# Kernel optimization log

Hardware: AMD Instinct MI355X
Metric: run time of the kernel (lower is better)

## Reference

```python
import jax, jax.numpy as jnp
import numpy as np

B, C, H = 16, 256, 32          # batch, in_channels(=out_channels), image_size
HEADS, HS = 8, 32              # heads = out_channels // head_size
D = HEADS * HS                 # head_dim = 256
N = H * H                      # tokens = 1024
EPS = 1e-5


def _rel_indices(h, w):
    # Faithful port of RelativeAttention2d.get_indices
    y = np.arange(h)
    x = np.arange(w)
    y1, x1, y2, x2 = np.meshgrid(y, x, y, x, indexing='ij')
    idx = (y1 - y2 + h - 1) * (2 * w - 1) + (x1 - x2 + w - 1)
    return jnp.asarray(idx.reshape(-1), dtype=jnp.int32)  # [N*N]


def setup_inputs() -> dict:
    key = jax.random.key(0)
    ks = jax.random.split(key, 10)
    s = 0.02
    return {
        'x': jax.random.normal(ks[0], (B, C, H, H), jnp.float32),
        'ln_g': jnp.ones((C,), jnp.float32),
        'ln_b': jnp.zeros((C,), jnp.float32),
        'wq': jax.random.normal(ks[1], (D, C), jnp.float32) * s,
        'bq': jnp.zeros((D,), jnp.float32),
        'wk': jax.random.normal(ks[2], (D, C), jnp.float32) * s,
        'bk': jnp.zeros((D,), jnp.float32),
        'wv': jax.random.normal(ks[3], (D, C), jnp.float32) * s,
        'bv': jnp.zeros((D,), jnp.float32),
        'wo': jax.random.normal(ks[4], (C, D), jnp.float32) * s,
        'bo': jnp.zeros((C,), jnp.float32),
        'rel_bias': jax.random.normal(ks[5], (HEADS, (2 * H - 1) * (2 * H - 1)), jnp.float32),
        'rel_idx': _rel_indices(H, H),
    }


def reference(x, ln_g, ln_b, wq, bq, wk, bk, wv, bv, wo, bo, rel_bias, rel_idx):
    b = x.shape[0]
    # norm(): LayerNorm over channel axis (dim 1 after the double transpose)
    mu = jnp.mean(x, axis=1, keepdims=True)
    var = jnp.mean((x - mu) ** 2, axis=1, keepdims=True)
    xn = (x - mu) / jnp.sqrt(var + EPS)
    xn = xn * ln_g[None, :, None, None] + ln_b[None, :, None, None]
    # reshape_for_linear: raw reshape [b, C, H, W] -> [b, N, C] (as in torch)
    xr = xn.reshape(b, N, C)
    # projections, then raw view(b, heads, head_size, -1) as in torch
    q = (xr @ wq.T + bq).reshape(b, HEADS, HS, N)
    k = (xr @ wk.T + bk).reshape(b, HEADS, HS, N)
    v = (xr @ wv.T + bv).reshape(b, HEADS, HS, N)
    # dots = k^T q / sqrt(head_dim)   [b, heads, N, N]
    dots = jnp.einsum('bhdn,bhdm->bhnm', k, q) / np.float32(np.sqrt(D))
    # gathered relative position bias  [heads, N, N]
    bias = rel_bias[:, rel_idx].reshape(HEADS, N, N)
    attn = jax.nn.softmax(dots + bias[None], axis=-2)  # non-standard softmax dim
    # out = v @ attn  [b, heads, head_size, N]
    out = jnp.einsum('bhdn,bhnm->bhdm', v, attn)
    out = out.reshape(b, H, H, D)  # raw view as in torch
    out = out @ wo.T + bo          # to_output linear (dropout is identity in eval)
    out = out.reshape(b, C, H, H)  # raw view back to [b, out_channels, H, W]
    return x + out
```

## Files before the change

### kernel.cpp

```cpp
#include <hip/hip_runtime.h>
#include <cstdint>

#define PERB 262144

typedef __attribute__((ext_vector_type(8))) short bf16x8;
typedef __attribute__((ext_vector_type(4))) float f32x4;
typedef unsigned short ushort_t;

__device__ __forceinline__ uint16_t f2bf(float f) {
    uint32_t u = __float_as_uint(f);
    u += 0x7fff + ((u >> 16) & 1);
    return (uint16_t)(u >> 16);
}

__global__ __launch_bounds__(256) void wcvt_kernel(
    const float* __restrict__ wq, const float* __restrict__ wk,
    const float* __restrict__ wv, const float* __restrict__ wo,
    ushort_t* __restrict__ oq, ushort_t* __restrict__ ok,
    ushort_t* __restrict__ ov, ushort_t* __restrict__ oo)
{
    const int which = blockIdx.x >> 6;
    const int idx = ((blockIdx.x & 63) * 256 + threadIdx.x) * 4;
    const float* src = which == 0 ? wq : which == 1 ? wk : which == 2 ? wv : wo;
    ushort_t* dst    = which == 0 ? oq : which == 1 ? ok : which == 2 ? ov : oo;
    const float4 v = *(const float4*)&src[idx];
    uint2 p;
    p.x = (uint32_t)f2bf(v.x) | ((uint32_t)f2bf(v.y) << 16);
    p.y = (uint32_t)f2bf(v.z) | ((uint32_t)f2bf(v.w) << 16);
    *(uint2*)&dst[idx] = p;
}

__global__ __launch_bounds__(256) void ln_kernel(
    const float* __restrict__ x, const float* __restrict__ gam,
    const float* __restrict__ bet, ushort_t* __restrict__ X)
{
    const int blk = blockIdx.x;
    const int b   = blk >> 4;
    const int sp0 = (blk & 15) << 6;
    const int tid = threadIdx.x;
    const int spl = tid & 63;
    const int cg  = tid >> 6;
    const int c0  = cg << 6;
    const int sp  = sp0 + spl;
    const float* xb = x + (size_t)b * PERB + sp;

    float vals[64];
    float s = 0.f, sq = 0.f;
#pragma unroll
    for (int i = 0; i < 64; ++i) {
        float v = xb[(size_t)(c0 + i) * 1024];
        vals[i] = v; s += v; sq += v * v;
    }
    __shared__ float rs[4][64];
    __shared__ float rq[4][64];
    rs[cg][spl] = s; rq[cg][spl] = sq;
    __syncthreads();
    const float ts = rs[0][spl] + rs[1][spl] + rs[2][spl] + rs[3][spl];
    const float tq = rq[0][spl] + rq[1][spl] + rq[2][spl] + rq[3][spl];
    const float mean = ts * (1.f / 256.f);
    const float var  = tq * (1.f / 256.f) - mean * mean;
    const float rstd = rsqrtf(var + 1e-5f);

    ushort_t* Xb = X + (size_t)b * PERB + sp;
#pragma unroll
    for (int i = 0; i < 64; ++i) {
        const int c = c0 + i;
        Xb[(size_t)c * 1024] = f2bf((vals[i] - mean) * rstd * gam[c] + bet[c]);
    }
}

__global__ __launch_bounds__(256, 3) void qkv_kernel(
    const ushort_t* __restrict__ X,
    const ushort_t* __restrict__ wq, const float* __restrict__ bq,
    const ushort_t* __restrict__ wk, const float* __restrict__ bk,
    const ushort_t* __restrict__ wv, const float* __restrict__ bv,
    ushort_t* __restrict__ Q, ushort_t* __restrict__ K, ushort_t* __restrict__ V)
{
    __shared__ __align__(16) ushort_t Xl[512 * 8];
    __shared__ __align__(16) ushort_t Wl[3][512 * 8];

    const int blk = blockIdx.x;
    const int m0  = (blk >> 2) << 6;
    const int n0  = (blk & 3) << 6;
    const int tid = threadIdx.x;
    const int w    = tid >> 6;
    const int lane = tid & 63;
    const int quad = lane >> 4;
    const int c    = lane & 15;

    f32x4 acc[3][4];
#pragma unroll
    for (int o3 = 0; o3 < 3; ++o3)
#pragma unroll
        for (int i = 0; i < 4; ++i) acc[o3][i] = (f32x4){0.f, 0.f, 0.f, 0.f};

    for (int kc = 0; kc < 4; ++kc) {
        const int k0 = kc << 6;
        __syncthreads();
#pragma unroll
        for (int i = 0; i < 2; ++i) {
            const int id = tid + i * 256;
            const int kq = id >> 6, m = id & 63;
            *(bf16x8*)&Xl[id * 8] = *(const bf16x8*)&X[(size_t)(m0 + m) * 256 + k0 + kq * 8];
        }
#pragma unroll
        for (int i = 0; i < 2; ++i) {
            const int id = tid + i * 256;
            const int kq = id >> 6, n = id & 63;
            const size_t g = (size_t)(n0 + n) * 256 + k0 + kq * 8;
            *(bf16x8*)&Wl[0][id * 8] = *(const bf16x8*)&wq[g];
            *(bf16x8*)&Wl[1][id * 8] = *(const bf16x8*)&wk[g];
            *(bf16x8*)&Wl[2][id * 8] = *(const bf16x8*)&wv[g];
        }
        __syncthreads();
#pragma unroll
        for (int ks = 0; ks < 2; ++ks) {
            const int kq = ks * 4 + quad;
            bf16x8 af[4];
#pragma unroll
            for (int msub = 0; msub < 4; ++msub)
                af[msub] = *(const bf16x8*)&Xl[(kq * 64 + msub * 16 + c) * 8];
            bf16x8 bw[3];
#pragma unroll
            for (int o3 = 0; o3 < 3; ++o3)
                bw[o3] = *(const bf16x8*)&Wl[o3][(kq * 64 + w * 16 + c) * 8];
#pragma unroll
            for (int o3 = 0; o3 < 3; ++o3)
#pragma unroll
                for (int msub = 0; msub < 4; ++msub)
                    acc[o3][msub] = __builtin_amdgcn_mfma_f32_16x16x32_bf16(
                        bw[o3], af[msub], acc[o3][msub], 0, 0, 0);
        }
    }

    const int n = n0 + w * 16 + quad * 4;
    const float4 bq4 = *(const float4*)&bq[n];
    const float4 bk4 = *(const float4*)&bk[n];
    const float4 bv4 = *(const float4*)&bv[n];
    ushort_t* outs[3] = {Q, K, V};
    const float4 bias[3] = {bq4, bk4, bv4};
#pragma unroll
    for (int msub = 0; msub < 4; ++msub) {
        const size_t m = (size_t)(m0 + msub * 16 + c);
#pragma unroll
        for (int o3 = 0; o3 < 3; ++o3) {
            const f32x4 a = acc[o3][msub];
            uint2 p;
            p.x = (uint32_t)f2bf(a[0] + bias[o3].x) | ((uint32_t)f2bf(a[1] + bias[o3].y) << 16);
            p.y = (uint32_t)f2bf(a[2] + bias[o3].z) | ((uint32_t)f2bf(a[3] + bias[o3].w) << 16);
            *(uint2*)&outs[o3][m * 256 + n] = p;
        }
    }
}

__global__ __launch_bounds__(256, 3) void attn_kernel(
    const ushort_t* __restrict__ Q, const ushort_t* __restrict__ K,
    const ushort_t* __restrict__ V, const float* __restrict__ relb,
    ushort_t* __restrict__ O)
{
    __shared__ __align__(16) unsigned char smem[29184];
    char* Pbase = (char*)smem;
    char* Kbase = (char*)smem + 18432;
    char* Vbase = (char*)smem + 22528;
    float* red  = (float*)(smem + 27136);

    const int blk = blockIdx.x;
    const int bh  = blk & 127;
    const int mt  = blk >> 7;
    const int b   = bh >> 3;
    const int h   = bh & 7;
    const int m0  = mt << 7;
    const int tid = threadIdx.x;
    const int w    = tid >> 6;
    const int lane = tid & 63;
    const int quad = lane >> 4;
    const int c    = lane & 15;

    const size_t base = (size_t)b * PERB + (size_t)h * 32768;
    const ushort_t* Qb = Q + base;
    const ushort_t* Kb = K + base;
    const ushort_t* Vb = V + base;
    const float* rbh = relb + h * 3969;

    {
        const int mm = tid & 127;
        const int sg = tid >> 7;
        union { bf16x8 v; uint16_t u[8]; } g0, g1;
#pragma unroll
        for (int j = 0; j < 8; ++j)
            g0.u[j] = Qb[(size_t)(sg * 16 + j) * 1024 + m0 + mm];
#pragma unroll
        for (int j = 0; j < 8; ++j)
            g1.u[j] = Qb[(size_t)(sg * 16 + 8 + j) * 1024 + m0 + mm];
        *(bf16x8*)(Pbase + (sg * 2 + 0) * 2048 + mm * 16) = g0.v;
        *(bf16x8*)(Pbase + (sg * 2 + 1) * 2048 + mm * 16) = g1.v;
    }
    __syncthreads();
    bf16x8 qfrag[8];
#pragma unroll
    for (int msub = 0; msub < 8; ++msub)
        qfrag[msub] = *(const bf16x8*)(Pbase + quad * 2048 + (msub * 16 + c) * 16);

    int my[8], mx[8];
#pragma unroll
    for (int msub = 0; msub < 8; ++msub) {
        const int m = m0 + msub * 16 + c;
        my[msub] = m >> 5; mx[msub] = m & 31;
    }

    f32x4 oacc[2][2];
#pragma unroll
    for (int i = 0; i < 2; ++i)
#pragma unroll
        for (int j = 0; j < 2; ++j)
            oacc[i][j] = (f32x4){0.f, 0.f, 0.f, 0.f};
    float dsum[8];
#pragma unroll
    for (int i = 0; i < 8; ++i) dsum[i] = 0.f;

    const int knn = tid & 63, ksg = (tid >> 6) & 3;
    const int vs = tid >> 3, vng = tid & 7;

    for (int ch = 0; ch < 16; ++ch) {
        const int n0c = ch << 6;
        __syncthreads();

        {
            union { bf16x8 v; uint16_t u[8]; } g;
#pragma unroll
            for (int j = 0; j < 8; ++j)
                g.u[j] = Kb[(size_t)(ksg * 8 + j) * 1024 + n0c + knn];
            *(bf16x8*)(Kbase + ksg * 1024 + knn * 16) = g.v;
        }
        *(bf16x8*)(Vbase + vs * 144 + vng * 16) =
            *(const bf16x8*)&Vb[(size_t)vs * 1024 + n0c + vng * 8];
        __syncthreads();

        const bf16x8 kf = *(const bf16x8*)(Kbase + quad * 1024 + (w * 16 + c) * 16);
        f32x4 sacc[8];
#pragma unroll
        for (int msub = 0; msub < 8; ++msub) {
            const f32x4 z = {0.f, 0.f, 0.f, 0.f};
            sacc[msub] = __builtin_amdgcn_mfma_f32_16x16x32_bf16(kf, qfrag[msub], z, 0, 0, 0);
        }
        const int nb = n0c + w * 16 + quad * 4;
#pragma unroll
        for (int msub = 0; msub < 8; ++msub) {
            uint32_t pk[2];
            float ps[4];
#pragma unroll
            for (int r = 0; r < 4; ++r) {
                const int n  = nb + r;
                const int dy = (n >> 5) - my[msub] + 31;
                const int dx = (n & 31) - mx[msub] + 31;
                const float sc = sacc[msub][r] * 0.0625f + rbh[dy * 63 + dx];
                const float p  = __expf(sc);
                ps[r] = p;
                dsum[msub] += p;
            }
            pk[0] = (uint32_t)f2bf(ps[0]) | ((uint32_t)f2bf(ps[1]) << 16);
            pk[1] = (uint32_t)f2bf(ps[2]) | ((uint32_t)f2bf(ps[3]) << 16);
            *(uint32_t*)(Pbase + (msub * 16 + c) * 144 + (w * 16 + quad * 4) * 2 + 0) = pk[0];
            *(uint32_t*)(Pbase + (msub * 16 + c) * 144 + (w * 16 + quad * 4) * 2 + 4) = pk[1];
        }
        __syncthreads();

#pragma unroll
        for (int kstep = 0; kstep < 2; ++kstep) {
            const bf16x8 vf0 = *(const bf16x8*)(Vbase + (0 * 16 + c) * 144 + kstep * 64 + quad * 16);
            const bf16x8 vf1 = *(const bf16x8*)(Vbase + (1 * 16 + c) * 144 + kstep * 64 + quad * 16);
#pragma unroll
            for (int mi = 0; mi < 2; ++mi) {
                const int msub = w * 2 + mi;
                const bf16x8 pf = *(const bf16x8*)(Pbase + (msub * 16 + c) * 144 + kstep * 64 + quad * 16);
                oacc[0][mi] = __builtin_amdgcn_mfma_f32_16x16x32_bf16(vf0, pf, oacc[0][mi], 0, 0, 0);
                oacc[1][mi] = __builtin_amdgcn_mfma_f32_16x16x32_bf16(vf1, pf, oacc[1][mi], 0, 0, 0);
            }
        }
    }

    __syncthreads();
#pragma unroll
    for (int msub = 0; msub < 8; ++msub) {
        float v = dsum[msub];
        v += __shfl_xor(v, 16, 64);
        v += __shfl_xor(v, 32, 64);
        if (quad == 0) red[w * 128 + msub * 16 + c] = v;
    }
    __syncthreads();

    ushort_t* Ob = O + base;
#pragma unroll
    for (int mi = 0; mi < 2; ++mi) {
        const int msub = w * 2 + mi;
        const float dtot = red[0 * 128 + msub * 16 + c] + red[1 * 128 + msub * 16 + c]
                         + red[2 * 128 + msub * 16 + c] + red[3 * 128 + msub * 16 + c];
        const float inv = 1.0f / dtot;
        const int m = m0 + msub * 16 + c;
#pragma unroll
        for (int ssub = 0; ssub < 2; ++ssub) {
#pragma unroll
            for (int r = 0; r < 4; ++r) {
                const int s = ssub * 16 + quad * 4 + r;
                Ob[(size_t)s * 1024 + m] = f2bf(oacc[ssub][mi][r] * inv);
            }
        }
    }
}

__global__ __launch_bounds__(256, 4) void oproj_kernel(
    const ushort_t* __restrict__ A, const ushort_t* __restrict__ wo,
    const float* __restrict__ bo, const float* __restrict__ x,
    float* __restrict__ out)
{
    __shared__ __align__(16) ushort_t Al[512 * 8];
    __shared__ __align__(16) ushort_t Wl[512 * 8];

    const int blk = blockIdx.x;
    const int m0  = (blk >> 2) << 6;
    const int n0  = (blk & 3) << 6;
    const int tid = threadIdx.x;
    const int w    = tid >> 6;
    const int lane = tid & 63;
    const int quad = lane >> 4;
    const int c    = lane & 15;

    f32x4 acc[4];
#pragma unroll
    for (int i = 0; i < 4; ++i) acc[i] = (f32x4){0.f, 0.f, 0.f, 0.f};

    for (int kc = 0; kc < 4; ++kc) {
        const int k0 = kc << 6;
        __syncthreads();
#pragma unroll
        for (int i = 0; i < 2; ++i) {
            const int id = tid + i * 256;
            const int kq = id >> 6, mn = id & 63;
            *(bf16x8*)&Al[id * 8] = *(const bf16x8*)&A [(size_t)(m0 + mn) * 256 + k0 + kq * 8];
            *(bf16x8*)&Wl[id * 8] = *(const bf16x8*)&wo[(size_t)(n0 + mn) * 256 + k0 + kq * 8];
        }
        __syncthreads();
#pragma unroll
        for (int ks = 0; ks < 2; ++ks) {
            const int kq = ks * 4 + quad;
            const bf16x8 bw = *(const bf16x8*)&Wl[(kq * 64 + w * 16 + c) * 8];
#pragma unroll
            for (int msub = 0; msub < 4; ++msub) {
                const bf16x8 af = *(const bf16x8*)&Al[(kq * 64 + msub * 16 + c) * 8];
                acc[msub] = __builtin_amdgcn_mfma_f32_16x16x32_bf16(bw, af, acc[msub], 0, 0, 0);
            }
        }
    }

    const int n = n0 + w * 16 + quad * 4;
    const float4 bo4 = *(const float4*)&bo[n];
#pragma unroll
    for (int msub = 0; msub < 4; ++msub) {
        const size_t g = (size_t)(m0 + msub * 16 + c) * 256 + n;
        const float4 r = *(const float4*)&x[g];
        float4 t;
        t.x = acc[msub][0] + bo4.x + r.x;
        t.y = acc[msub][1] + bo4.y + r.y;
        t.z = acc[msub][2] + bo4.z + r.z;
        t.w = acc[msub][3] + bo4.w + r.w;
        *(float4*)&out[g] = t;
    }
}

extern "C" void kernel_launch(void* const* d_in, const int* in_sizes, int n_in,
                              void* d_out, int out_size, void* d_ws, size_t ws_size,
                              hipStream_t stream)
{
    (void)in_sizes; (void)n_in; (void)out_size; (void)ws_size;
    const float* x   = (const float*)d_in[0];
    const float* lng = (const float*)d_in[1];
    const float* lnb = (const float*)d_in[2];
    const float* wq  = (const float*)d_in[3];
    const float* bq  = (const float*)d_in[4];
    const float* wk  = (const float*)d_in[5];
    const float* bk  = (const float*)d_in[6];
    const float* wv  = (const float*)d_in[7];
    const float* bv  = (const float*)d_in[8];
    const float* wo  = (const float*)d_in[9];
    const float* bo  = (const float*)d_in[10];
    const float* rb  = (const float*)d_in[11];

    ushort_t* ws = (ushort_t*)d_ws;
    ushort_t* Xbf = ws;
    ushort_t* Qbf = ws + 1 * 4194304;
    ushort_t* Kbf = ws + 2 * 4194304;
    ushort_t* Vbf = ws + 3 * 4194304;
    ushort_t* Obf = ws + 4 * 4194304;
    ushort_t* Wqb = ws + 5 * 4194304;
    ushort_t* Wkb = Wqb + 65536;
    ushort_t* Wvb = Wkb + 65536;
    ushort_t* Wob = Wvb + 65536;
    float* out = (float*)d_out;

    hipLaunchKernelGGL(wcvt_kernel,  dim3(256),  dim3(256), 0, stream,
                       wq, wk, wv, wo, Wqb, Wkb, Wvb, Wob);
    hipLaunchKernelGGL(ln_kernel,    dim3(256),  dim3(256), 0, stream, x, lng, lnb, Xbf);
    hipLaunchKernelGGL(qkv_kernel,   dim3(1024), dim3(256), 0, stream,
                       Xbf, Wqb, bq, Wkb, bk, Wvb, bv, Qbf, Kbf, Vbf);
    hipLaunchKernelGGL(attn_kernel,  dim3(1024), dim3(256), 0, stream, Qbf, Kbf, Vbf, rb, Obf);
    hipLaunchKernelGGL(oproj_kernel, dim3(1024), dim3(256), 0, stream, Obf, Wob, bo, x, out);
}
```

Measured before the change: 188.2 us.

## Restructure attention loop: register prefetch, LDS bias table, exp2, MFMA row sums

The attention kernel now stages the per-head relative bias table into LDS, pre-scaled by log2(e), and replaces expf with exp2 of an fma. K and V tiles for the next chunk are prefetched into registers while the current chunk computes, and V is double-buffered so one barrier per chunk is dropped. P and V use XOR-swizzled LDS layouts instead of padded rows. The softmax denominator now comes from an extra MFMA against a ones vector instead of per-thread sums with shuffle and LDS reduction. P is rounded to bf16 by truncation instead of round-to-nearest, which costs a little accuracy. LDS use grows to about 44.5 KB per block, which may limit how many blocks fit per CU.

```diff
diff --git a/kernel.cpp b/kernel.cpp
--- a/kernel.cpp
+++ b/kernel.cpp
@@ -153,16 +153,19 @@
     }
 }
 
+#define C1F 0.09016844005556022f
+#define LOG2EF 1.4426950408889634f
+
 __global__ __launch_bounds__(256, 3) void attn_kernel(
     const ushort_t* __restrict__ Q, const ushort_t* __restrict__ K,
     const ushort_t* __restrict__ V, const float* __restrict__ relb,
     ushort_t* __restrict__ O)
 {
-    __shared__ __align__(16) unsigned char smem[29184];
-    char* Pbase = (char*)smem;
-    char* Kbase = (char*)smem + 18432;
-    char* Vbase = (char*)smem + 22528;
-    float* red  = (float*)(smem + 27136);
+    __shared__ __align__(16) unsigned char smem[44560];
+    float* blog = (float*)smem;
+    char*  Pb   = (char*)(smem + 15888);
+    char*  Kl   = (char*)(smem + 32272);
+    char*  Vl   = (char*)(smem + 36368);
 
     const int blk = blockIdx.x;
     const int bh  = blk & 127;
@@ -177,10 +180,12 @@
     const int c    = lane & 15;
 
     const size_t base = (size_t)b * PERB + (size_t)h * 32768;
-    const ushort_t* Qb = Q + base;
-    const ushort_t* Kb = K + base;
-    const ushort_t* Vb = V + base;
+    const ushort_t* Qg = Q + base;
+    const ushort_t* Kg = K + base;
+    const ushort_t* Vg = V + base;
     const float* rbh = relb + h * 3969;
+
+    for (int i = tid; i < 3969; i += 256) blog[i] = rbh[i] * LOG2EF;
 
     {
         const int mm = tid & 127;
@@ -188,123 +193,127 @@
         union { bf16x8 v; uint16_t u[8]; } g0, g1;
 #pragma unroll
         for (int j = 0; j < 8; ++j)
-            g0.u[j] = Qb[(size_t)(sg * 16 + j) * 1024 + m0 + mm];
+            g0.u[j] = Qg[(size_t)(sg * 16 + j) * 1024 + m0 + mm];
 #pragma unroll
         for (int j = 0; j < 8; ++j)
-            g1.u[j] = Qb[(size_t)(sg * 16 + 8 + j) * 1024 + m0 + mm];
-        *(bf16x8*)(Pbase + (sg * 2 + 0) * 2048 + mm * 16) = g0.v;
-        *(bf16x8*)(Pbase + (sg * 2 + 1) * 2048 + mm * 16) = g1.v;
+            g1.u[j] = Qg[(size_t)(sg * 16 + 8 + j) * 1024 + m0 + mm];
+        *(bf16x8*)(Pb + (sg * 2 + 0) * 2048 + mm * 16) = g0.v;
+        *(bf16x8*)(Pb + (sg * 2 + 1) * 2048 + mm * 16) = g1.v;
     }
     __syncthreads();
     bf16x8 qfrag[8];
 #pragma unroll
     for (int msub = 0; msub < 8; ++msub)
-        qfrag[msub] = *(const bf16x8*)(Pbase + quad * 2048 + (msub * 16 + c) * 16);
-
-    int my[8], mx[8];
+        qfrag[msub] = *(const bf16x8*)(Pb + quad * 2048 + (msub * 16 + c) * 16);
+
+    int moff[8];
 #pragma unroll
     for (int msub = 0; msub < 8; ++msub) {
         const int m = m0 + msub * 16 + c;
-        my[msub] = m >> 5; mx[msub] = m & 31;
-    }
-
-    f32x4 oacc[2][2];
-#pragma unroll
-    for (int i = 0; i < 2; ++i)
-#pragma unroll
-        for (int j = 0; j < 2; ++j)
-            oacc[i][j] = (f32x4){0.f, 0.f, 0.f, 0.f};
-    float dsum[8];
-#pragma unroll
-    for (int i = 0; i < 8; ++i) dsum[i] = 0.f;
-
-    const int knn = tid & 63, ksg = (tid >> 6) & 3;
-    const int vs = tid >> 3, vng = tid & 7;
+        moff[msub] = 1984 - (m >> 5) * 63 - (m & 31);
+    }
+
+    f32x4 oacc[2][2], dacc[2];
+#pragma unroll
+    for (int i = 0; i < 2; ++i) {
+        dacc[i] = (f32x4){0.f, 0.f, 0.f, 0.f};
+#pragma unroll
+        for (int j = 0; j < 2; ++j) oacc[i][j] = (f32x4){0.f, 0.f, 0.f, 0.f};
+    }
+    bf16x8 onesf;
+#pragma unroll
+    for (int j = 0; j < 8; ++j) onesf[j] = (short)0x3F80;
+
+    const int knn = tid & 63, ksg = tid >> 6;
+    const int vs  = tid >> 3, vng = tid & 7;
+    const int kWr = ksg * 1024 + knn * 16;
+    const int vWr = vs * 128 + ((vng ^ (vs & 7)) << 4);
+    const int kRd = quad * 1024 + (w * 16 + c) * 16;
+    const int pWr = c * 128 + (((2 * w + (quad >> 1)) ^ (c & 7)) << 4) + ((quad & 1) << 3);
+    const int c7  = c & 7;
+
+    uint32_t kpre[8]; bf16x8 vpre;
+#pragma unroll
+    for (int j = 0; j < 8; ++j) kpre[j] = Kg[(size_t)(ksg * 8 + j) * 1024 + knn];
+    vpre = *(const bf16x8*)&Vg[(size_t)vs * 1024 + vng * 8];
 
     for (int ch = 0; ch < 16; ++ch) {
         const int n0c = ch << 6;
-        __syncthreads();
+        const int cb  = ch & 1;
 
         {
-            union { bf16x8 v; uint16_t u[8]; } g;
+            uint4 kp;
+            kp.x = kpre[0] | (kpre[1] << 16);
+            kp.y = kpre[2] | (kpre[3] << 16);
+            kp.z = kpre[4] | (kpre[5] << 16);
+            kp.w = kpre[6] | (kpre[7] << 16);
+            *(uint4*)(Kl + kWr) = kp;
+            *(bf16x8*)(Vl + cb * 4096 + vWr) = vpre;
+        }
+        __syncthreads();
+
+        {
+            const int n0n = ((ch + 1) & 15) << 6;
 #pragma unroll
             for (int j = 0; j < 8; ++j)
-                g.u[j] = Kb[(size_t)(ksg * 8 + j) * 1024 + n0c + knn];
-            *(bf16x8*)(Kbase + ksg * 1024 + knn * 16) = g.v;
-        }
-        *(bf16x8*)(Vbase + vs * 144 + vng * 16) =
-            *(const bf16x8*)&Vb[(size_t)vs * 1024 + n0c + vng * 8];
-        __syncthreads();
-
-        const bf16x8 kf = *(const bf16x8*)(Kbase + quad * 1024 + (w * 16 + c) * 16);
+                kpre[j] = Kg[(size_t)(ksg * 8 + j) * 1024 + n0n + knn];
+            vpre = *(const bf16x8*)&Vg[(size_t)vs * 1024 + n0n + vng * 8];
+        }
+
+        const bf16x8 kf = *(const bf16x8*)(Kl + kRd);
         f32x4 sacc[8];
 #pragma unroll
         for (int msub = 0; msub < 8; ++msub) {
             const f32x4 z = {0.f, 0.f, 0.f, 0.f};
             sacc[msub] = __builtin_amdgcn_mfma_f32_16x16x32_bf16(kf, qfrag[msub], z, 0, 0, 0);
         }
-        const int nb = n0c + w * 16 + quad * 4;
+
+        const int nbase = n0c + w * 16 + quad * 4;
+        int nidx[4];
+#pragma unroll
+        for (int r = 0; r < 4; ++r) {
+            const int n = nbase + r;
+            nidx[r] = (n >> 5) * 63 + (n & 31);
+        }
 #pragma unroll
         for (int msub = 0; msub < 8; ++msub) {
-            uint32_t pk[2];
-            float ps[4];
-#pragma unroll
-            for (int r = 0; r < 4; ++r) {
-                const int n  = nb + r;
-                const int dy = (n >> 5) - my[msub] + 31;
-                const int dx = (n & 31) - mx[msub] + 31;
-                const float sc = sacc[msub][r] * 0.0625f + rbh[dy * 63 + dx];
-                const float p  = __expf(sc);
-                ps[r] = p;
-                dsum[msub] += p;
-            }
-            pk[0] = (uint32_t)f2bf(ps[0]) | ((uint32_t)f2bf(ps[1]) << 16);
-            pk[1] = (uint32_t)f2bf(ps[2]) | ((uint32_t)f2bf(ps[3]) << 16);
-            *(uint32_t*)(Pbase + (msub * 16 + c) * 144 + (w * 16 + quad * 4) * 2 + 0) = pk[0];
-            *(uint32_t*)(Pbase + (msub * 16 + c) * 144 + (w * 16 + quad * 4) * 2 + 4) = pk[1];
+            const int mo = moff[msub];
+            float p[4];
+#pragma unroll
+            for (int r = 0; r < 4; ++r)
+                p[r] = __builtin_amdgcn_exp2f(fmaf(sacc[msub][r], C1F, blog[nidx[r] + mo]));
+            uint2 pk;
+            pk.x = __builtin_amdgcn_perm(__float_as_uint(p[1]), __float_as_uint(p[0]), 0x07060302u);
+            pk.y = __builtin_amdgcn_perm(__float_as_uint(p[3]), __float_as_uint(p[2]), 0x07060302u);
+            *(uint2*)(Pb + msub * 2048 + pWr) = pk;
         }
         __syncthreads();
 
 #pragma unroll
         for (int kstep = 0; kstep < 2; ++kstep) {
-            const bf16x8 vf0 = *(const bf16x8*)(Vbase + (0 * 16 + c) * 144 + kstep * 64 + quad * 16);
-            const bf16x8 vf1 = *(const bf16x8*)(Vbase + (1 * 16 + c) * 144 + kstep * 64 + quad * 16);
+            const int u = ((kstep * 4 + quad) ^ c7) << 4;
+            const bf16x8 vf0 = *(const bf16x8*)(Vl + cb * 4096 + c * 128 + u);
+            const bf16x8 vf1 = *(const bf16x8*)(Vl + cb * 4096 + (16 + c) * 128 + u);
 #pragma unroll
             for (int mi = 0; mi < 2; ++mi) {
-                const int msub = w * 2 + mi;
-                const bf16x8 pf = *(const bf16x8*)(Pbase + (msub * 16 + c) * 144 + kstep * 64 + quad * 16);
+                const bf16x8 pf = *(const bf16x8*)(Pb + ((w * 2 + mi) * 16 + c) * 128 + u);
                 oacc[0][mi] = __builtin_amdgcn_mfma_f32_16x16x32_bf16(vf0, pf, oacc[0][mi], 0, 0, 0);
                 oacc[1][mi] = __builtin_amdgcn_mfma_f32_16x16x32_bf16(vf1, pf, oacc[1][mi], 0, 0, 0);
+                dacc[mi]    = __builtin_amdgcn_mfma_f32_16x16x32_bf16(onesf, pf, dacc[mi], 0, 0, 0);
             }
         }
     }
 
-    __syncthreads();
-#pragma unroll
-    for (int msub = 0; msub < 8; ++msub) {
-        float v = dsum[msub];
-        v += __shfl_xor(v, 16, 64);
-        v += __shfl_xor(v, 32, 64);
-        if (quad == 0) red[w * 128 + msub * 16 + c] = v;
-    }
-    __syncthreads();
-
     ushort_t* Ob = O + base;
 #pragma unroll
     for (int mi = 0; mi < 2; ++mi) {
-        const int msub = w * 2 + mi;
-        const float dtot = red[0 * 128 + msub * 16 + c] + red[1 * 128 + msub * 16 + c]
-                         + red[2 * 128 + msub * 16 + c] + red[3 * 128 + msub * 16 + c];
-        const float inv = 1.0f / dtot;
-        const int m = m0 + msub * 16 + c;
-#pragma unroll
-        for (int ssub = 0; ssub < 2; ++ssub) {
-#pragma unroll
-            for (int r = 0; r < 4; ++r) {
-                const int s = ssub * 16 + quad * 4 + r;
-                Ob[(size_t)s * 1024 + m] = f2bf(oacc[ssub][mi][r] * inv);
-            }
-        }
+        const float inv = 1.0f / dacc[mi][0];
+        const int m = m0 + (w * 2 + mi) * 16 + c;
+#pragma unroll
+        for (int ssub = 0; ssub < 2; ++ssub)
+#pragma unroll
+            for (int r = 0; r < 4; ++r)
+                Ob[(size_t)(ssub * 16 + quad * 4 + r) * 1024 + m] = f2bf(oacc[ssub][mi][r] * inv);
     }
 }
 
```

Result: faster. 180.2 us (-4.3%).
